# Performance work log

Measured on AMD Instinct MI355X. Metric: run time of the kernel, lower is better.

Reference implementation:

```python
import jax, jax.numpy as jnp
import numpy as np

D_MODEL = 1024
D_STATE = 16
D_CONV = 4
EXPAND = 2
D_INNER = D_MODEL * EXPAND          # 2048
DT_RANK = max(1, D_MODEL // 16)     # 64
BATCH, SEQ = 4, 2048


def setup_inputs() -> dict:
    key = jax.random.key(0)
    ks = jax.random.split(key, 8)
    s = lambda n: 1.0 / np.sqrt(n)
    x = jax.random.normal(ks[0], (BATCH, SEQ, D_MODEL), jnp.float32)
    in_proj_w = jax.random.normal(ks[1], (2 * D_INNER, D_MODEL), jnp.float32) * s(D_MODEL)
    conv_w = jax.random.normal(ks[2], (D_INNER, 1, D_CONV), jnp.float32) * s(D_CONV)
    conv_b = jax.random.normal(ks[3], (D_INNER,), jnp.float32) * 0.01
    x_proj_w = jax.random.normal(ks[4], (DT_RANK + 2 * D_STATE, D_INNER), jnp.float32) * s(D_INNER)
    dt_proj_w = jax.random.normal(ks[5], (D_INNER, DT_RANK), jnp.float32) * s(DT_RANK)
    dt_proj_b = jax.random.normal(ks[6], (D_INNER,), jnp.float32) * 0.01
    A_log = jnp.broadcast_to(jnp.log(jnp.arange(1, D_STATE + 1, dtype=jnp.float32))[None, :],
                             (D_INNER, D_STATE)).copy()
    D_param = jnp.ones((D_INNER,), jnp.float32)
    out_proj_w = jax.random.normal(ks[7], (D_MODEL, D_INNER), jnp.float32) * s(D_INNER)
    return {"x": x, "in_proj_w": in_proj_w, "conv_w": conv_w, "conv_b": conv_b,
            "x_proj_w": x_proj_w, "dt_proj_w": dt_proj_w, "dt_proj_b": dt_proj_b,
            "A_log": A_log, "D_param": D_param, "out_proj_w": out_proj_w}


def _ssm_forward(x, in_proj_w, conv_w, conv_b, x_proj_w, dt_proj_w, dt_proj_b,
                 A_log, D_param, out_proj_w):
    B, L, _ = x.shape
    # input projection -> (B, L, 2*D_INNER), split into x_ssm and gate z
    xz = jnp.einsum('bld,ed->ble', x, in_proj_w)
    x_ssm, z = xz[..., :D_INNER], xz[..., D_INNER:]
    # causal depthwise conv1d (torch pads both sides then slices [:L] == left pad only)
    xc = jnp.transpose(x_ssm, (0, 2, 1))  # (B, D_INNER, L)
    xc = jax.lax.conv_general_dilated(
        xc, conv_w, window_strides=(1,), padding=[(D_CONV - 1, 0)],
        dimension_numbers=('NCH', 'OIH', 'NCH'), feature_group_count=D_INNER)
    xc = xc + conv_b[None, :, None]
    x_ssm = jax.nn.silu(jnp.transpose(xc, (0, 2, 1)))  # (B, L, D_INNER)
    # input-dependent dt, B, C
    dbl = jnp.einsum('bld,ed->ble', x_ssm, x_proj_w)  # (B, L, DT_RANK+2N)
    dt_x = dbl[..., :DT_RANK]
    B_x = dbl[..., DT_RANK:DT_RANK + D_STATE]
    C_x = dbl[..., DT_RANK + D_STATE:]
    dt = jax.nn.softplus(jnp.einsum('blr,dr->bld', dt_x, dt_proj_w) + dt_proj_b)  # (B, L, D_INNER)
    A = -jnp.exp(A_log)  # (D_INNER, D_STATE)

    # selective scan over L with lax.scan; carry h: (B, D_INNER, D_STATE)
    def step(h, inp):
        dt_t, B_t, C_t, x_t = inp  # (B,D), (B,N), (B,N), (B,D)
        dA = jnp.exp(dt_t[:, :, None] * A[None, :, :])          # (B, D, N)
        dB = dt_t[:, :, None] * B_t[:, None, :]                 # (B, D, N)
        h = dA * h + dB * x_t[:, :, None]
        y_t = jnp.einsum('bdn,bn->bd', h, C_t)
        return h, y_t

    h0 = jnp.zeros((B, D_INNER, D_STATE), x.dtype)
    xs = (jnp.moveaxis(dt, 1, 0), jnp.moveaxis(B_x, 1, 0),
          jnp.moveaxis(C_x, 1, 0), jnp.moveaxis(x_ssm, 1, 0))
    _, ys = jax.lax.scan(step, h0, xs)          # ys: (L, B, D_INNER)
    y = jnp.moveaxis(ys, 0, 1) + D_param[None, None, :] * x_ssm
    y = y * jax.nn.silu(z)
    return jnp.einsum('ble,de->bld', y, out_proj_w)


def reference(x, in_proj_w, conv_w, conv_b, x_proj_w, dt_proj_w, dt_proj_b,
              A_log, D_param, out_proj_w):
    return _ssm_forward(x, in_proj_w, conv_w, conv_b, x_proj_w, dt_proj_w,
                        dt_proj_b, A_log, D_param, out_proj_w)
```

## Files before the change

kernel.cpp:

```cpp
#include <hip/hip_runtime.h>
#include <hip/hip_bf16.h>
#include <math.h>

#define D_MODEL 1024
#define D_STATE 16
#define D_CONV 4
#define D_INNER 2048
#define DT_RANK 64
#define BATCH 4
#define SEQ 2048
#define ML (BATCH * SEQ)
#define NCH 64
#define CL (SEQ / NCH)

typedef __attribute__((ext_vector_type(8))) short short8;
typedef __attribute__((ext_vector_type(8))) unsigned short u16x8;
typedef __attribute__((ext_vector_type(4))) float f32x4;

__device__ __forceinline__ float bf2f(unsigned short u) {
  union { unsigned int i; float f; } v;
  v.i = ((unsigned int)u) << 16;
  return v.f;
}
__device__ __forceinline__ unsigned short f2bf(float f) {
  union { float f; unsigned int i; } u;
  u.f = f;
  unsigned int r = u.i + 0x7fffu + ((u.i >> 16) & 1u);
  return (unsigned short)(r >> 16);
}
__device__ __forceinline__ unsigned int f2bf_pk(float a, float b) {
  union { __hip_bfloat162 h; unsigned int u; } cv;
  cv.h = __float22bfloat162_rn(make_float2(a, b));
  return cv.u;
}
template <bool BF>
__device__ __forceinline__ float ld1(const void* p, size_t i) {
  if constexpr (BF) return bf2f(((const unsigned short*)p)[i]);
  else return ((const float*)p)[i];
}
template <bool BF>
__device__ __forceinline__ void ld4(const void* p, size_t i, float o[4]) {
  if constexpr (BF) {
    ushort4 v = *(const ushort4*)((const unsigned short*)p + i);
    o[0] = bf2f(v.x); o[1] = bf2f(v.y); o[2] = bf2f(v.z); o[3] = bf2f(v.w);
  } else {
    float4 v = *(const float4*)((const float*)p + i);
    o[0] = v.x; o[1] = v.y; o[2] = v.z; o[3] = v.w;
  }
}

__device__ __forceinline__ void gl_lds16(const unsigned short* g,
                                         unsigned short* l) {
  __builtin_amdgcn_global_load_lds(
      (const __attribute__((address_space(1))) void*)g,
      (__attribute__((address_space(3))) void*)l, 16, 0, 0);
}

__global__ void detect_kernel(const unsigned int* __restrict__ xw, int* flag) {
  __shared__ int cnt;
  if (threadIdx.x == 0) cnt = 0;
  __syncthreads();
  unsigned int w = xw[threadIdx.x];
  unsigned int e = (w >> 7) & 0xffu;
  if (e < 100u || e > 145u) atomicAdd(&cnt, 1);
  __syncthreads();
  if (threadIdx.x == 0) flag[0] = (cnt < 32) ? 1 : 0;
}

#define CVT_N0 (ML * 1024)
#define CVT_N1 (4096 * 1024)
#define CVT_N2 (1024 * 2048)
#define CVT_N3 (2048 * 64)
#define CVT_N4 (128 * 2048)
#define CVT_E0 CVT_N0
#define CVT_E1 (CVT_E0 + CVT_N1)
#define CVT_E2 (CVT_E1 + CVT_N2)
#define CVT_E3 (CVT_E2 + CVT_N3)
#define CVT_E4 (CVT_E3 + CVT_N4)

__device__ __forceinline__ void cvt4(const void* in, size_t i,
                                     unsigned short* out, size_t o, int bf) {
  if (bf) {
    *(ushort4*)(out + o) = *(const ushort4*)((const unsigned short*)in + i);
  } else {
    float4 f = *(const float4*)((const float*)in + i);
    uint2 v;
    v.x = f2bf_pk(f.x, f.y);
    v.y = f2bf_pk(f.z, f.w);
    *(uint2*)(out + o) = v;
  }
}

__global__ __launch_bounds__(256) void cvt_all_kernel(
    const void* __restrict__ x, const void* __restrict__ ipw,
    const void* __restrict__ opw, const void* __restrict__ dtw,
    const void* __restrict__ xpw, unsigned short* __restrict__ x_bf,
    unsigned short* __restrict__ ipw_bf, unsigned short* __restrict__ opw_bf,
    unsigned short* __restrict__ dtw_bf, unsigned short* __restrict__ xpw_pad,
    const int* __restrict__ flag) {
  const int bf = *flag;
  const size_t g = (size_t)(blockIdx.x * 256 + threadIdx.x) * 4;
  if (g < CVT_E0) {
    cvt4(x, g, x_bf, g, bf);
  } else if (g < CVT_E1) {
    const size_t i = g - CVT_E0;
    cvt4(ipw, i, ipw_bf, i, bf);
  } else if (g < CVT_E2) {
    const size_t i = g - CVT_E1;
    cvt4(opw, i, opw_bf, i, bf);
  } else if (g < CVT_E3) {
    const size_t i = g - CVT_E2;
    cvt4(dtw, i, dtw_bf, i, bf);
  } else if (g < CVT_E4) {
    const size_t i = g - CVT_E3;
    const int row = (int)(i >> 11);
    if (row < 96) {
      cvt4(xpw, i, xpw_pad, i, bf);
    } else {
      ushort4 z = {0, 0, 0, 0};
      *(ushort4*)(xpw_pad + i) = z;
    }
  }
}

#define K1_LDA 1024
#define K1_NT 16

#define K1_STG(srcbase, lds, t_, h_)                                       \
  {                                                                        \
    const unsigned short* s_ =                                             \
        (srcbase) + (size_t)(h_) * (128 * K1_LDA) + (size_t)(t_) * 64;     \
    unsigned short* d_ = (lds) + (((t_) & 1) * 2 + (h_)) * 8192 + w * 512; \
    gl_lds16(s_, d_);                                                      \
    gl_lds16(s_ + 64 * K1_LDA, d_ + 4096);                                 \
  }

__global__ __launch_bounds__(512, 2) void gemm256_k1(
    const unsigned short* __restrict__ A,
    const unsigned short* __restrict__ B,
    unsigned short* __restrict__ C) {
  __shared__ unsigned short As[32768];
  __shared__ unsigned short Bs[32768];
  const int tid = threadIdx.x;
  const int l = tid & 63, w = tid >> 6;
  const int bid = blockIdx.x;
  const int swz = (bid & 7) * 64 + (bid >> 3);
  const int m0 = (swz >> 4) * 256, n0 = (swz & 15) * 256;
  const int row0 = tid >> 3;
  const int c0 = (tid & 7) ^ (row0 & 7);
  const unsigned short* aSrc = A + (size_t)(m0 + row0) * K1_LDA + c0 * 8;
  const unsigned short* bSrc = B + (size_t)(n0 + row0) * K1_LDA + c0 * 8;
  const int q = l >> 4, mr = l & 15;
  const int wm = w >> 2, wn = w & 3;

  K1_STG(aSrc, As, 0, 0);
  K1_STG(aSrc, As, 0, 1);
  K1_STG(bSrc, Bs, 0, 0);
  K1_STG(bSrc, Bs, 0, 1);
  K1_STG(bSrc, Bs, 1, 0);
  K1_STG(bSrc, Bs, 1, 1);
  K1_STG(aSrc, As, 1, 0);
  asm volatile("s_waitcnt vmcnt(6)" ::: "memory");
  asm volatile("s_barrier" ::: "memory");

  f32x4 acc[8][4] = {};
  for (int t = 0; t < K1_NT; ++t) {
    const int tb = (t & 1) * 2;
    short8 bfr[4][2];
#pragma unroll
    for (int ni = 0; ni < 4; ++ni)
#pragma unroll
      for (int kk = 0; kk < 2; ++kk) {
        const int r = (wn & 1) * 64 + ni * 16 + mr;
        const int c = kk * 4 + q;
        bfr[ni][kk] = *(const short8*)&Bs[(tb + (wn >> 1)) * 8192 + r * 64 +
                                          ((c ^ (r & 7)) * 8)];
      }
#pragma unroll
    for (int p = 0; p < 4; ++p) {
      short8 af[2][2];
#pragma unroll
      for (int i = 0; i < 2; ++i)
#pragma unroll
        for (int kk = 0; kk < 2; ++kk) {
          const int r = (2 * p + i) * 16 + mr;
          const int c = kk * 4 + q;
          af[i][kk] = *(const short8*)&As[(tb + wm) * 8192 + r * 64 +
                                          ((c ^ (r & 7)) * 8)];
        }
      if (p == 0) {
        if (t + 1 < K1_NT) K1_STG(aSrc, As, t + 1, 1);
      } else if (p == 1) {
        if (t + 2 < K1_NT) K1_STG(bSrc, Bs, t + 2, 0);
      } else if (p == 2) {
        if (t + 2 < K1_NT) K1_STG(bSrc, Bs, t + 2, 1);
      } else {
        if (t + 2 < K1_NT) K1_STG(aSrc, As, t + 2, 0);
      }
      asm volatile("s_barrier" ::: "memory");
      __builtin_amdgcn_s_setprio(1);
#pragma unroll
      for (int i = 0; i < 2; ++i)
#pragma unroll
        for (int ni = 0; ni < 4; ++ni)
#pragma unroll
          for (int kk = 0; kk < 2; ++kk)
            acc[2 * p + i][ni] = __builtin_amdgcn_mfma_f32_16x16x32_bf16(
                af[i][kk], bfr[ni][kk], acc[2 * p + i][ni], 0, 0, 0);
      __builtin_amdgcn_s_setprio(0);
      if (p == 3) {
        if (t + 2 < K1_NT) {
          asm volatile("s_waitcnt vmcnt(6)" ::: "memory");
        } else {
          asm volatile("s_waitcnt vmcnt(0)" ::: "memory");
        }
      }
      asm volatile("s_barrier" ::: "memory");
    }
  }
#pragma unroll
  for (int mi = 0; mi < 8; ++mi) {
#pragma unroll
    for (int ni = 0; ni < 4; ++ni) {
      const int row = m0 + wm * 128 + mi * 16 + q * 4;
      const int col = n0 + wn * 64 + ni * 16 + mr;
      const size_t off0 = (size_t)row * 4096 + col;
      const unsigned int p01 = f2bf_pk(acc[mi][ni][0], acc[mi][ni][1]);
      const unsigned int p23 = f2bf_pk(acc[mi][ni][2], acc[mi][ni][3]);
      C[off0] = (unsigned short)p01;
      C[off0 + 4096] = (unsigned short)(p01 >> 16);
      C[off0 + 2 * 4096] = (unsigned short)p23;
      C[off0 + 3 * 4096] = (unsigned short)(p23 >> 16);
    }
  }
}

template <int EPI, int TAG>
__global__ __launch_bounds__(256) void gemm_mfma(
    const unsigned short* __restrict__ Ain, int lda,
    const unsigned short* __restrict__ Bin, int ldb, void* __restrict__ C,
    int ldc, int K, const void* __restrict__ bias,
    const int* __restrict__ flag) {
  __shared__ unsigned short As[128 * 32];
  __shared__ unsigned short Bs[128 * 32];
  const unsigned short* A = Ain;
  const unsigned short* B = Bin;
  if (EPI == 3) {
    A += (size_t)blockIdx.z * 512;
    B += (size_t)blockIdx.z * 512;
  }
  const int tid = threadIdx.x;
  const int l = tid & 63, w = tid >> 6;
  const int bm = blockIdx.y * 128;
  const int bn = blockIdx.x * 128;
  const int r0 = w * 16 + (l >> 2);
  const int cc = (((l & 3) ^ ((l >> 2) & 3) ^ ((l >> 4) & 3))) * 8;
  const unsigned short* Ap0 = A + (size_t)(bm + r0) * lda + cc;
  const unsigned short* Ap1 = A + (size_t)(bm + r0 + 64) * lda + cc;
  const unsigned short* Bp0 = B + (size_t)(bn + r0) * ldb + cc;
  const unsigned short* Bp1 = B + (size_t)(bn + r0 + 64) * ldb + cc;
  const int q = l >> 4, mr = l & 15;
  const int wm = w >> 1, wn = w & 1;
  const int slot = (q ^ (mr & 3) ^ (mr >> 2)) * 8;
  f32x4 acc[4][4] = {};
  for (int k0 = 0; k0 < K; k0 += 32) {
    gl_lds16(Ap0 + k0, As + w * 512);
    gl_lds16(Ap1 + k0, As + 2048 + w * 512);
    gl_lds16(Bp0 + k0, Bs + w * 512);
    gl_lds16(Bp1 + k0, Bs + 2048 + w * 512);
    __syncthreads();
    short8 af[4], bfr[4];
#pragma unroll
    for (int mi = 0; mi < 4; ++mi)
      af[mi] = *(const short8*)&As[(wm * 64 + mi * 16 + mr) * 32 + slot];
#pragma unroll
    for (int ni = 0; ni < 4; ++ni)
      bfr[ni] = *(const short8*)&Bs[(wn * 64 + ni * 16 + mr) * 32 + slot];
#pragma unroll
    for (int mi = 0; mi < 4; ++mi)
#pragma unroll
      for (int ni = 0; ni < 4; ++ni)
        acc[mi][ni] = __builtin_amdgcn_mfma_f32_16x16x32_bf16(
            af[mi], bfr[ni], acc[mi][ni], 0, 0, 0);
    __syncthreads();
  }
  const int bf = (EPI == 1 || EPI == 2) ? *flag : 0;
  float* Cp3 = (EPI == 3)
                   ? ((float*)C + (size_t)blockIdx.z * ML * 128)
                   : (float*)C;
#pragma unroll
  for (int mi = 0; mi < 4; ++mi) {
#pragma unroll
    for (int ni = 0; ni < 4; ++ni) {
      const int row = bm + wm * 64 + mi * 16 + q * 4;
      const int col = bn + wn * 64 + ni * 16 + mr;
      const size_t off0 = (size_t)row * ldc + col;
      if (EPI == 0) {
        const unsigned int p01 = f2bf_pk(acc[mi][ni][0], acc[mi][ni][1]);
        const unsigned int p23 = f2bf_pk(acc[mi][ni][2], acc[mi][ni][3]);
        unsigned short* C16 = (unsigned short*)C;
        C16[off0] = (unsigned short)p01;
        C16[off0 + ldc] = (unsigned short)(p01 >> 16);
        C16[off0 + 2 * (size_t)ldc] = (unsigned short)p23;
        C16[off0 + 3 * (size_t)ldc] = (unsigned short)(p23 >> 16);
      } else if (EPI == 3) {
#pragma unroll
        for (int j = 0; j < 4; ++j)
          Cp3[off0 + (size_t)j * ldc] = acc[mi][ni][j];
      } else if (EPI == 2) {
        float v[4];
        const float bv = bf ? ld1<true>(bias, col) : ld1<false>(bias, col);
#pragma unroll
        for (int j = 0; j < 4; ++j) {
          const float t = acc[mi][ni][j] + bv;
          v[j] = fmaxf(t, 0.f) + __logf(1.f + __expf(-fabsf(t)));
        }
        const unsigned int p01 = f2bf_pk(v[0], v[1]);
        const unsigned int p23 = f2bf_pk(v[2], v[3]);
        unsigned short* C16 = (unsigned short*)C;
        C16[off0] = (unsigned short)p01;
        C16[off0 + ldc] = (unsigned short)(p01 >> 16);
        C16[off0 + 2 * (size_t)ldc] = (unsigned short)p23;
        C16[off0 + 3 * (size_t)ldc] = (unsigned short)(p23 >> 16);
      } else {
        if (bf) {
          const unsigned int p01 = f2bf_pk(acc[mi][ni][0], acc[mi][ni][1]);
          const unsigned int p23 = f2bf_pk(acc[mi][ni][2], acc[mi][ni][3]);
          unsigned short* C16 = (unsigned short*)C;
          C16[off0] = (unsigned short)p01;
          C16[off0 + ldc] = (unsigned short)(p01 >> 16);
          C16[off0 + 2 * (size_t)ldc] = (unsigned short)p23;
          C16[off0 + 3 * (size_t)ldc] = (unsigned short)(p23 >> 16);
        } else {
          float* Cf = (float*)C;
#pragma unroll
          for (int j = 0; j < 4; ++j)
            Cf[off0 + (size_t)j * ldc] = acc[mi][ni][j];
        }
      }
    }
  }
}

__global__ __launch_bounds__(256) void reduceK3_kernel(
    const float* __restrict__ part, unsigned short* __restrict__ dbl) {
  const size_t i = (size_t)(blockIdx.x * 256 + threadIdx.x) * 4;
  const size_t st = (size_t)ML * 128;
  float4 a = *(const float4*)(part + i);
  float4 b = *(const float4*)(part + st + i);
  float4 c = *(const float4*)(part + 2 * st + i);
  float4 d = *(const float4*)(part + 3 * st + i);
  uint2 v;
  v.x = f2bf_pk(a.x + b.x + c.x + d.x, a.y + b.y + c.y + d.y);
  v.y = f2bf_pk(a.z + b.z + c.z + d.z, a.w + b.w + c.w + d.w);
  *(uint2*)(dbl + i) = v;
}

__global__ __launch_bounds__(256) void conv_silu_kernel(
    const unsigned short* __restrict__ xzb, const void* __restrict__ cw,
    const void* __restrict__ cb, unsigned short* __restrict__ xcb,
    const int* __restrict__ flag) {
  const int bf = *flag;
  const int e = (blockIdx.x * 256 + threadIdx.x) * 4;
  const int d = e & (D_INNER - 1);
  const int bl = e >> 11;
  const int l = bl & (SEQ - 1);
  const size_t base = (size_t)bl * 4096 + d;
  float x0[4], x1[4] = {}, x2[4] = {}, x3[4] = {};
  ld4<true>(xzb, base, x0);
  if (l >= 1) ld4<true>(xzb, base - 4096, x1);
  if (l >= 2) ld4<true>(xzb, base - 2 * 4096, x2);
  if (l >= 3) ld4<true>(xzb, base - 3 * 4096, x3);
  float r[4];
#pragma unroll
  for (int i = 0; i < 4; ++i) {
    float w[4];
    if (bf) ld4<true>(cw, (size_t)(d + i) * 4, w);
    else ld4<false>(cw, (size_t)(d + i) * 4, w);
    const float bias = bf ? ld1<true>(cb, d + i) : ld1<false>(cb, d + i);
    float acc = bias + w[3] * x0[i] + w[2] * x1[i] + w[1] * x2[i] + w[0] * x3[i];
    r[i] = acc / (1.f + __expf(-acc));
  }
  uint2 o;
  o.x = f2bf_pk(r[0], r[1]);
  o.y = f2bf_pk(r[2], r[3]);
  *(uint2*)(xcb + e) = o;
}

__device__ __forceinline__ void load_a(const void* A_log, int bf, int d,
                                       float a[16], float& dev) {
  float t[4];
#pragma unroll
  for (int k = 0; k < 4; ++k) {
    if (bf) ld4<true>(A_log, (size_t)d * 16 + k * 4, t);
    else ld4<false>(A_log, (size_t)d * 16 + k * 4, t);
#pragma unroll
    for (int j = 0; j < 4; ++j) a[k * 4 + j] = -expf(t[j]);
  }
  dev = 0.f;
#pragma unroll
  for (int n = 0; n < 16; ++n) dev = fmaxf(dev, fabsf(a[n] + (float)(n + 1)));
}

__device__ __forceinline__ void pow_tree(float e1, float pw[16]) {
  const float e2 = e1 * e1;
  const float e3 = e2 * e1;
  const float e4 = e2 * e2;
  pw[0] = e1; pw[1] = e2; pw[2] = e3; pw[3] = e4;
  pw[4] = e4 * e1; pw[5] = e4 * e2; pw[6] = e4 * e3; pw[7] = e4 * e4;
  const float e8 = pw[7];
  pw[8] = e8 * e1; pw[9] = e8 * e2; pw[10] = e8 * e3; pw[11] = e8 * e4;
  pw[12] = e8 * pw[4]; pw[13] = e8 * pw[5]; pw[14] = e8 * pw[6];
  pw[15] = e8 * e8;
}

__global__ __launch_bounds__(256) void scan_passA(
    const unsigned short* __restrict__ xzb,
    const unsigned short* __restrict__ xcb,
    const unsigned short* __restrict__ dbl, const void* __restrict__ A_log,
    const int* __restrict__ flag, float* __restrict__ S,
    float* __restrict__ P) {
  const int bf = *flag;
  const int gid = blockIdx.x * 256 + threadIdx.x;
  const int d = gid & (D_INNER - 1);
  const int c = (gid >> 11) & (NCH - 1);
  const int b = gid >> 17;
  float a[16], dev;
  load_a(A_log, bf, d, a, dev);
  float h[16] = {};
  float sdt = 0.f;
  const size_t m0 = (size_t)b * SEQ + c * CL;
  if (dev < 1e-3f) {
    for (int t = 0; t < CL; ++t) {
      const size_t m = m0 + t;
      const float dtv = bf2f(xzb[m * 4096 + d]);
      const float xv = bf2f(xcb[m * 2048 + d]);
      const u16x8 B0 = *(const u16x8*)&dbl[m * 128 + 64];
      const u16x8 B1 = *(const u16x8*)&dbl[m * 128 + 72];
      const float dtx = dtv * xv;
      sdt += dtv;
      float pw[16];
      pow_tree(__expf(-dtv), pw);
#pragma unroll
      for (int n = 0; n < 16; ++n) {
        const float Bv = bf2f(n < 8 ? B0[n] : B1[n - 8]);
        h[n] = fmaf(pw[n], h[n], Bv * dtx);
      }
    }
  } else {
    for (int t = 0; t < CL; ++t) {
      const size_t m = m0 + t;
      const float dtv = bf2f(xzb[m * 4096 + d]);
      const float xv = bf2f(xcb[m * 2048 + d]);
      const u16x8 B0 = *(const u16x8*)&dbl[m * 128 + 64];
      const u16x8 B1 = *(const u16x8*)&dbl[m * 128 + 72];
      const float dtx = dtv * xv;
      sdt += dtv;
#pragma unroll
      for (int n = 0; n < 16; ++n) {
        const float Bv = bf2f(n < 8 ? B0[n] : B1[n - 8]);
        h[n] = fmaf(__expf(dtv * a[n]), h[n], Bv * dtx);
      }
    }
  }
  const size_t sidx = (((size_t)b * NCH + c) * D_INNER + d) * 16;
#pragma unroll
  for (int n = 0; n < 16; ++n) {
    S[sidx + n] = h[n];
    P[sidx + n] = __expf(a[n] * sdt);
  }
}

__global__ __launch_bounds__(256) void scan_passB(float* __restrict__ S,
                                                  const float* __restrict__ P) {
  const int idx = blockIdx.x * 256 + threadIdx.x;
  const int n = idx & 15;
  const int d = (idx >> 4) & (D_INNER - 1);
  const int b = idx >> 15;
  float h = 0.f;
  for (int c = 0; c < NCH; ++c) {
    const size_t sidx = (((size_t)b * NCH + c) * D_INNER + d) * 16 + n;
    const float s = S[sidx], p = P[sidx];
    S[sidx] = h;
    h = p * h + s;
  }
}

__global__ __launch_bounds__(256) void scan_passC(
    const unsigned short* __restrict__ xzb,
    const unsigned short* __restrict__ xcb,
    const unsigned short* __restrict__ dbl, const void* __restrict__ A_log,
    const void* __restrict__ Dp, const float* __restrict__ S,
    const int* __restrict__ flag, unsigned short* __restrict__ ybf) {
  const int bf = *flag;
  const int gid = blockIdx.x * 256 + threadIdx.x;
  const int d = gid & (D_INNER - 1);
  const int c = (gid >> 11) & (NCH - 1);
  const int b = gid >> 17;
  float a[16], dev;
  load_a(A_log, bf, d, a, dev);
  const float Dv = bf ? ld1<true>(Dp, d) : ld1<false>(Dp, d);
  float h[16];
  const size_t sidx = (((size_t)b * NCH + c) * D_INNER + d) * 16;
#pragma unroll
  for (int n = 0; n < 16; ++n) h[n] = S[sidx + n];
  const size_t m0 = (size_t)b * SEQ + c * CL;
  const bool trick = dev < 1e-3f;
  for (int t = 0; t < CL; ++t) {
    const size_t m = m0 + t;
    const float dtv = bf2f(xzb[m * 4096 + d]);
    const float xv = bf2f(xcb[m * 2048 + d]);
    const u16x8 B0 = *(const u16x8*)&dbl[m * 128 + 64];
    const u16x8 B1 = *(const u16x8*)&dbl[m * 128 + 72];
    const u16x8 C0 = *(const u16x8*)&dbl[m * 128 + 80];
    const u16x8 C1 = *(const u16x8*)&dbl[m * 128 + 88];
    const float dtx = dtv * xv;
    float y = 0.f;
    if (trick) {
      float pw[16];
      pow_tree(__expf(-dtv), pw);
#pragma unroll
      for (int n = 0; n < 16; ++n) {
        const float Bv = bf2f(n < 8 ? B0[n] : B1[n - 8]);
        const float Cv = bf2f(n < 8 ? C0[n] : C1[n - 8]);
        h[n] = fmaf(pw[n], h[n], Bv * dtx);
        y = fmaf(h[n], Cv, y);
      }
    } else {
#pragma unroll
      for (int n = 0; n < 16; ++n) {
        const float Bv = bf2f(n < 8 ? B0[n] : B1[n - 8]);
        const float Cv = bf2f(n < 8 ? C0[n] : C1[n - 8]);
        h[n] = fmaf(__expf(dtv * a[n]), h[n], Bv * dtx);
        y = fmaf(h[n], Cv, y);
      }
    }
    const float zv = bf2f(xzb[m * 4096 + 2048 + d]);
    const float yv = y + Dv * xv;
    ybf[m * 2048 + d] = f2bf(yv * (zv / (1.f + __expf(-zv))));
  }
}

extern "C" void kernel_launch(void* const* d_in, const int* in_sizes, int n_in,
                              void* d_out, int out_size, void* d_ws,
                              size_t ws_size, hipStream_t stream) {
  const void* x = d_in[0];
  const void* in_proj_w = d_in[1];
  const void* conv_w = d_in[2];
  const void* conv_b = d_in[3];
  const void* x_proj_w = d_in[4];
  const void* dt_proj_w = d_in[5];
  const void* dt_proj_b = d_in[6];
  const void* A_log = d_in[7];
  const void* D_param = d_in[8];
  const void* out_proj_w = d_in[9];

  char* wsb = (char*)d_ws;
  int* flag = (int*)wsb;
  unsigned short* xzb = (unsigned short*)(wsb + 256);
  unsigned short* xcb = xzb + (size_t)ML * 4096;
  unsigned short* dbl = xcb + (size_t)ML * 2048;
  unsigned short* ybf = dbl + (size_t)ML * 128;
  float* S = (float*)(ybf + (size_t)ML * 2048);
  float* P = S + (size_t)BATCH * NCH * D_INNER * 16;
  unsigned short* opw_bf =
      (unsigned short*)(P + (size_t)BATCH * NCH * D_INNER * 16);
  unsigned short* xpw_pad = opw_bf + (size_t)1024 * 2048;
  unsigned short* dtw_bf = xpw_pad + (size_t)128 * 2048;
  unsigned short* x_bf = xcb;
  unsigned short* ipw_bf = xcb + (size_t)ML * 1024;
  float* k3part = S;

  detect_kernel<<<1, 256, 0, stream>>>((const unsigned int*)x, flag);
  cvt_all_kernel<<<CVT_E4 / 1024, 256, 0, stream>>>(
      x, in_proj_w, out_proj_w, dt_proj_w, x_proj_w, x_bf, ipw_bf, opw_bf,
      dtw_bf, xpw_pad, flag);
  gemm256_k1<<<dim3(512), 512, 0, stream>>>(x_bf, ipw_bf, xzb);
  conv_silu_kernel<<<(ML * D_INNER) / 1024, 256, 0, stream>>>(
      xzb, conv_w, conv_b, xcb, flag);
  {
    dim3 g(1, ML / 128, 4);
    gemm_mfma<3, 3><<<g, 256, 0, stream>>>(xcb, 2048, xpw_pad, 2048, k3part,
                                           128, 512, nullptr, flag);
  }
  reduceK3_kernel<<<(ML * 128) / 1024, 256, 0, stream>>>(k3part, dbl);
  {
    dim3 g(2048 / 128, ML / 128);
    gemm_mfma<2, 4><<<g, 256, 0, stream>>>(dbl, 128, dtw_bf, 64, xzb, 4096,
                                           64, dt_proj_b, flag);
  }
  scan_passA<<<(BATCH * NCH * D_INNER) / 256, 256, 0, stream>>>(
      xzb, xcb, dbl, A_log, flag, S, P);
  scan_passB<<<(BATCH * D_INNER * 16) / 256, 256, 0, stream>>>(S, P);
  scan_passC<<<(BATCH * NCH * D_INNER) / 256, 256, 0, stream>>>(
      xzb, xcb, dbl, A_log, D_param, S, flag, ybf);
  {
    dim3 g(1024 / 128, ML / 128);
    gemm_mfma<1, 6><<<g, 256, 0, stream>>>(ybf, 2048, opw_bf, 2048, d_out,
                                           1024, 2048, nullptr, flag);
  }
}
```

Measured before the change: 480.1 us.

## Add dedicated dt-projection GEMM with reused B tile and pipelined A staging

```diff
diff --git a/kernel.cpp b/kernel.cpp
--- a/kernel.cpp
+++ b/kernel.cpp
@@ -235,6 +235,103 @@
   }
 }
 
+__global__ __launch_bounds__(256) void dt_gemm_kernel(
+    const unsigned short* __restrict__ Adbl,
+    const unsigned short* __restrict__ Bw,
+    unsigned short* __restrict__ Cdt,
+    const void* __restrict__ bias, const int* __restrict__ flag) {
+  __shared__ unsigned short Bs[128 * 64];
+  __shared__ unsigned short Ass[4][128 * 64];
+  const int tid = threadIdx.x;
+  const int l = tid & 63, w = tid >> 6;
+  const int bn = blockIdx.x * 128;
+  const int mg = blockIdx.y * 512;
+  const int srow = tid >> 3;
+  const int sc = ((tid & 7) ^ (srow & 7)) * 8;
+  const unsigned short* aSrc = Adbl + (size_t)(mg + srow) * 128 + sc;
+  const unsigned short* bSrc = Bw + (size_t)(bn + srow) * 64 + sc;
+#define K4_STGB(i_) gl_lds16(bSrc + (i_) * 32 * 64, Bs + (i_)*2048 + w * 512)
+#define K4_STGA(mt_, i_)                                  \
+  gl_lds16(aSrc + (size_t)((mt_)*128 + (i_)*32) * 128,    \
+           Ass[(mt_) & 3] + (i_)*2048 + w * 512)
+  K4_STGB(0); K4_STGB(1); K4_STGB(2); K4_STGB(3);
+  K4_STGA(0, 0); K4_STGA(0, 1); K4_STGA(0, 2); K4_STGA(0, 3);
+  K4_STGA(1, 0); K4_STGA(1, 1); K4_STGA(1, 2); K4_STGA(1, 3);
+  asm volatile("s_waitcnt vmcnt(4)" ::: "memory");
+  asm volatile("s_barrier" ::: "memory");
+  const int q = l >> 4, mr = l & 15;
+  const int wm = w >> 1, wn = w & 1;
+  short8 bfr[4][2];
+#pragma unroll
+  for (int ni = 0; ni < 4; ++ni)
+#pragma unroll
+    for (int kk = 0; kk < 2; ++kk) {
+      const int r = wn * 64 + ni * 16 + mr;
+      const int c = kk * 4 + q;
+      bfr[ni][kk] = *(const short8*)&Bs[r * 64 + ((c ^ (r & 7)) * 8)];
+    }
+  const int bf = *flag;
+  float bv[4];
+#pragma unroll
+  for (int ni = 0; ni < 4; ++ni) {
+    const int col = bn + wn * 64 + ni * 16 + mr;
+    bv[ni] = bf ? ld1<true>(bias, col) : ld1<false>(bias, col);
+  }
+#pragma unroll
+  for (int mt = 0; mt < 4; ++mt) {
+    if (mt + 2 < 4) {
+      K4_STGA(mt + 2, 0); K4_STGA(mt + 2, 1);
+      K4_STGA(mt + 2, 2); K4_STGA(mt + 2, 3);
+    }
+    short8 af[4][2];
+#pragma unroll
+    for (int mi = 0; mi < 4; ++mi)
+#pragma unroll
+      for (int kk = 0; kk < 2; ++kk) {
+        const int r = wm * 64 + mi * 16 + mr;
+        const int c = kk * 4 + q;
+        af[mi][kk] =
+            *(const short8*)&Ass[mt & 3][r * 64 + ((c ^ (r & 7)) * 8)];
+      }
+    f32x4 acc[4][4] = {};
+#pragma unroll
+    for (int mi = 0; mi < 4; ++mi)
+#pragma unroll
+      for (int ni = 0; ni < 4; ++ni)
+#pragma unroll
+        for (int kk = 0; kk < 2; ++kk)
+          acc[mi][ni] = __builtin_amdgcn_mfma_f32_16x16x32_bf16(
+              af[mi][kk], bfr[ni][kk], acc[mi][ni], 0, 0, 0);
+#pragma unroll
+    for (int mi = 0; mi < 4; ++mi) {
+#pragma unroll
+      for (int ni = 0; ni < 4; ++ni) {
+        const int row = mg + mt * 128 + wm * 64 + mi * 16 + q * 4;
+        const int col = bn + wn * 64 + ni * 16 + mr;
+        const size_t off0 = (size_t)row * 4096 + col;
+        float v[4];
+#pragma unroll
+        for (int j = 0; j < 4; ++j) {
+          const float t = acc[mi][ni][j] + bv[ni];
+          v[j] = fmaxf(t, 0.f) + __logf(1.f + __expf(-fabsf(t)));
+        }
+        const unsigned int p01 = f2bf_pk(v[0], v[1]);
+        const unsigned int p23 = f2bf_pk(v[2], v[3]);
+        Cdt[off0] = (unsigned short)p01;
+        Cdt[off0 + 4096] = (unsigned short)(p01 >> 16);
+        Cdt[off0 + 2 * 4096] = (unsigned short)p23;
+        Cdt[off0 + 3 * 4096] = (unsigned short)(p23 >> 16);
+      }
+    }
+    if (mt + 2 < 4) {
+      asm volatile("s_waitcnt vmcnt(4)" ::: "memory");
+    } else {
+      asm volatile("s_waitcnt vmcnt(0)" ::: "memory");
+    }
+    if (mt < 3) asm volatile("s_barrier" ::: "memory");
+  }
+}
+
 template <int EPI, int TAG>
 __global__ __launch_bounds__(256) void gemm_mfma(
     const unsigned short* __restrict__ Ain, int lda,
@@ -284,7 +381,7 @@
             af[mi], bfr[ni], acc[mi][ni], 0, 0, 0);
     __syncthreads();
   }
-  const int bf = (EPI == 1 || EPI == 2) ? *flag : 0;
+  const int bf = (EPI == 1) ? *flag : 0;
   float* Cp3 = (EPI == 3)
                    ? ((float*)C + (size_t)blockIdx.z * ML * 128)
                    : (float*)C;
@@ -307,21 +404,6 @@
 #pragma unroll
         for (int j = 0; j < 4; ++j)
           Cp3[off0 + (size_t)j * ldc] = acc[mi][ni][j];
-      } else if (EPI == 2) {
-        float v[4];
-        const float bv = bf ? ld1<true>(bias, col) : ld1<false>(bias, col);
-#pragma unroll
-        for (int j = 0; j < 4; ++j) {
-          const float t = acc[mi][ni][j] + bv;
-          v[j] = fmaxf(t, 0.f) + __logf(1.f + __expf(-fabsf(t)));
-        }
-        const unsigned int p01 = f2bf_pk(v[0], v[1]);
-        const unsigned int p23 = f2bf_pk(v[2], v[3]);
-        unsigned short* C16 = (unsigned short*)C;
-        C16[off0] = (unsigned short)p01;
-        C16[off0 + ldc] = (unsigned short)(p01 >> 16);
-        C16[off0 + 2 * (size_t)ldc] = (unsigned short)p23;
-        C16[off0 + 3 * (size_t)ldc] = (unsigned short)(p23 >> 16);
       } else {
         if (bf) {
           const unsigned int p01 = f2bf_pk(acc[mi][ni][0], acc[mi][ni][1]);
@@ -584,11 +666,8 @@
                                            128, 512, nullptr, flag);
   }
   reduceK3_kernel<<<(ML * 128) / 1024, 256, 0, stream>>>(k3part, dbl);
-  {
-    dim3 g(2048 / 128, ML / 128);
-    gemm_mfma<2, 4><<<g, 256, 0, stream>>>(dbl, 128, dtw_bf, 64, xzb, 4096,
-                                           64, dt_proj_b, flag);
-  }
+  dt_gemm_kernel<<<dim3(16, 16), 256, 0, stream>>>(dbl, dtw_bf, xzb,
+                                                   dt_proj_b, flag);
   scan_passA<<<(BATCH * NCH * D_INNER) / 256, 256, 0, stream>>>(
       xzb, xcb, dbl, A_log, flag, S, P);
   scan_passB<<<(BATCH * D_INNER * 16) / 256, 256, 0, stream>>>(S, P);
```

After: 484.1 us. About the same (+0.8%).
